# Optimization experiments

Measured on AMD Instinct MI355X. Metric: run time of the kernel, lower is better.

## Reference

```python
import jax, jax.numpy as jnp
import numpy as np

EMBED = 256      # embedding_dim
HEADS = 4        # attn_heads
OUT = EMBED // HEADS  # out_channels per head = 64
R = 8            # n_relations = len(metapaths) + 1
N = 16384        # num_nodes
NEG_SLOPE = 0.2  # PyG GATv2 default leaky_relu slope


def setup_inputs() -> dict:
    key = jax.random.key(0)
    ks = jax.random.split(key, 16)
    s = 0.05
    inp = {"relation_embs": jax.random.normal(ks[0], (N, R, EMBED), jnp.float32)}
    # Two GATv2Conv layers: lin_l (src), lin_r (dst), att vector, output bias.
    for i in range(2):
        inp[f"Wl{i}"] = jax.random.normal(ks[1 + 6 * i], (EMBED, HEADS, OUT), jnp.float32) * s
        inp[f"bl{i}"] = jax.random.normal(ks[2 + 6 * i], (HEADS, OUT), jnp.float32) * s
        inp[f"Wr{i}"] = jax.random.normal(ks[3 + 6 * i], (EMBED, HEADS, OUT), jnp.float32) * s
        inp[f"br{i}"] = jax.random.normal(ks[4 + 6 * i], (HEADS, OUT), jnp.float32) * s
        inp[f"att{i}"] = jax.random.normal(ks[5 + 6 * i], (HEADS, OUT), jnp.float32) * s
        inp[f"bias{i}"] = jax.random.normal(ks[6 + 6 * i], (HEADS * OUT,), jnp.float32) * s
    return inp


def reference(relation_embs, Wl0, bl0, Wr0, br0, att0, bias0,
              Wl1, bl1, Wr1, br1, att1, bias1):
    # Each node owns a fully-connected graph over its R relation embeddings
    # (all rows nonzero under randn fill), so the PyG gather/softmax/scatter
    # collapses to dense [N, R_dst, R_src] attention.
    h = jax.nn.relu(relation_embs)                                  # [N,R,D]

    # ---- GATv2 layer 0: full FC edges (every src -> every dst) ----
    xl = jnp.einsum('nrd,dhc->nrhc', h, Wl0) + bl0                  # src feats [N,R,H,C]
    xr = jnp.einsum('nrd,dhc->nrhc', h, Wr0) + br0                  # dst feats [N,R,H,C]
    e = jax.nn.leaky_relu(xr[:, :, None] + xl[:, None], NEG_SLOPE)  # [N,Ri,Rj,H,C]
    logits = jnp.einsum('nijhc,hc->nijh', e, att0)                  # [N,Ri,Rj,H]
    alpha = jax.nn.softmax(logits, axis=2)                          # softmax over src j
    h = jnp.einsum('nijh,njhc->nihc', alpha, xl)                    # [N,R,H,C]
    h = h.reshape(N, R, HEADS * OUT) + bias0
    h = jax.nn.relu(h)

    # ---- GATv2 layer 1 (last): only edges into the self node (nid == R-1) ----
    xl = jnp.einsum('nrd,dhc->nrhc', h, Wl1) + bl1                  # src feats [N,R,H,C]
    xr_self = jnp.einsum('nd,dhc->nhc', h[:, -1], Wr1) + br1        # dst = self [N,H,C]
    e = jax.nn.leaky_relu(xr_self[:, None] + xl, NEG_SLOPE)         # [N,R,H,C]
    logits = jnp.einsum('nrhc,hc->nrh', e, att1)                    # [N,R,H]
    alpha = jax.nn.softmax(logits, axis=1)                          # softmax over src r
    out = jnp.einsum('nrh,nrhc->nhc', alpha, xl).reshape(N, HEADS * OUT) + bias1
    node_embs = jax.nn.relu(out)                                    # [N, D]

    # betas: last-layer attention into the self node, detached (SparseTensor.to_dense().detach())
    betas = jax.lax.stop_gradient(alpha)                            # [N,R,H]
    return node_embs, betas
```

## Files before the change

kernel.cpp:

```cpp
#include <hip/hip_runtime.h>


#define NNODES 16384
#define NB 8
#define MR 64

typedef __bf16 bf16x8 __attribute__((ext_vector_type(8)));
typedef __bf16 bf16x4 __attribute__((ext_vector_type(4)));
typedef float f32x4 __attribute__((ext_vector_type(4)));
typedef float f32x8 __attribute__((ext_vector_type(8)));

__device__ __forceinline__ int swz(int row, int chunk) {
    return row * 256 + ((chunk ^ (row & 7)) << 3);
}

__global__ void prep_weights(const float* __restrict__ Wl0, const float* __restrict__ Wr0,
                             const float* __restrict__ Wl1, const float* __restrict__ Wr1,
                             __bf16* __restrict__ wt) {
    __shared__ float tile[64 * 68];
    const int t  = threadIdx.x;
    const int m  = blockIdx.x >> 4;
    const int kt = (blockIdx.x >> 2) & 3;
    const int nt = blockIdx.x & 3;
    const float* src = (m == 0 ? Wl0 : m == 1 ? Wr0 : m == 2 ? Wl1 : Wr1) + kt * 64 * 256;
    #pragma unroll
    for (int i = 0; i < 4; ++i) {
        const int idx = i * 256 + t;
        const int kk  = idx >> 4;
        const int nn  = (idx & 15) * 4;
        const float4 v = *(const float4*)&src[kk * 256 + nt * 64 + nn];
        tile[kk * 68 + nn + 0] = v.x;
        tile[kk * 68 + nn + 1] = v.y;
        tile[kk * 68 + nn + 2] = v.z;
        tile[kk * 68 + nn + 3] = v.w;
    }
    __syncthreads();
    const int n  = t >> 2;
    const int ks = (t & 3) * 16;
    bf16x8 o0, o1;
    #pragma unroll
    for (int e = 0; e < 8; ++e) o0[e] = (__bf16)tile[(ks + e) * 68 + n];
    #pragma unroll
    for (int e = 0; e < 8; ++e) o1[e] = (__bf16)tile[(ks + 8 + e) * 68 + n];
    __bf16* dst = &wt[(size_t)(m * 256 + nt * 64 + n) * 256 + kt * 64 + ks];
    *(bf16x8*)dst = o0;
    *(bf16x8*)(dst + 8) = o1;
}

__launch_bounds__(512, 4)
__global__ void gat_fused(const float* __restrict__ x,
                          const float* __restrict__ bl0, const float* __restrict__ br0,
                          const float* __restrict__ att0, const float* __restrict__ bias0,
                          const float* __restrict__ bl1, const float* __restrict__ br1,
                          const float* __restrict__ att1, const float* __restrict__ bias1,
                          const __bf16* __restrict__ wt,
                          float* __restrict__ out) {
    __shared__ __bf16 bufA[MR * 256];
    __shared__ __bf16 bufB[MR * 256];
    __shared__ float attbuf[2560];

    const int tid  = threadIdx.x;
    const int bg   = blockIdx.x;
    const int lane = tid & 63;
    const int wv   = tid >> 6;
    const int lr   = lane & 15;
    const int lq   = lane >> 4;

    {
        const float4* src = (const float4*)(x + (size_t)bg * (MR * 256));
        #pragma unroll
        for (int it = 0; it < 4; ++it) {
            const int g   = it * 512 + tid;
            const int row = g >> 5;
            const int c   = g & 31;
            const float4 v0 = src[2 * g];
            const float4 v1 = src[2 * g + 1];
            bf16x8 s;
            s[0] = (__bf16)fmaxf(v0.x, 0.f); s[1] = (__bf16)fmaxf(v0.y, 0.f);
            s[2] = (__bf16)fmaxf(v0.z, 0.f); s[3] = (__bf16)fmaxf(v0.w, 0.f);
            s[4] = (__bf16)fmaxf(v1.x, 0.f); s[5] = (__bf16)fmaxf(v1.y, 0.f);
            s[6] = (__bf16)fmaxf(v1.z, 0.f); s[7] = (__bf16)fmaxf(v1.w, 0.f);
            *(bf16x8*)&bufA[swz(row, c)] = s;
        }
        if (tid < 256) attbuf[2048 + tid] = att0[tid];
        else           attbuf[2048 + tid] = att1[tid - 256];
    }
    __syncthreads();

    {
        f32x4 acc[4][4];
        #pragma unroll
        for (int m = 0; m < 4; ++m)
            #pragma unroll
            for (int n = 0; n < 4; ++n)
                acc[m][n] = f32x4{0.f, 0.f, 0.f, 0.f};
        #pragma unroll
        for (int kt = 0; kt < 8; ++kt) {
            bf16x8 a[4], b[4];
            #pragma unroll
            for (int m = 0; m < 4; ++m)
                a[m] = *(const bf16x8*)&bufA[swz(m * 16 + lr, kt * 4 + lq)];
            const int koff = kt * 32 + lq * 8;
            #pragma unroll
            for (int n = 0; n < 4; ++n)
                b[n] = *(const bf16x8*)&wt[(size_t)(wv * 64 + n * 16 + lr) * 256 + koff];
            #pragma unroll
            for (int m = 0; m < 4; ++m)
                #pragma unroll
                for (int n = 0; n < 4; ++n)
                    acc[m][n] = __builtin_amdgcn_mfma_f32_16x16x32_bf16(a[m], b[n], acc[m][n], 0, 0, 0);
        }
        __syncthreads();
        __bf16* dstbuf = (wv < 4) ? bufB : bufA;
        const float* bv = (wv < 4) ? bl0 : br0;
        #pragma unroll
        for (int n = 0; n < 4; ++n) {
            const int cl   = (wv & 3) * 64 + n * 16 + lr;
            const float bias = bv[cl];
            const int ch   = cl >> 3, ce = cl & 7;
            #pragma unroll
            for (int m = 0; m < 4; ++m)
                #pragma unroll
                for (int r = 0; r < 4; ++r) {
                    const int row = m * 16 + lq * 4 + r;
                    dstbuf[swz(row, ch) + ce] = (__bf16)(acc[m][n][r] + bias);
                }
        }
    }
    __syncthreads();

    {
        const int n  = tid >> 6;
        const int i  = (tid >> 3) & 7;
        const int h  = (tid >> 1) & 3;
        const int jh = tid & 1;
        const int rowR = n * 8 + i;
        float lg[4] = {0.f, 0.f, 0.f, 0.f};
        #pragma unroll
        for (int cc = 0; cc < 8; ++cc) {
            const bf16x8 vr = *(const bf16x8*)&bufA[swz(rowR, h * 8 + cc)];
            const f32x8 xr = __builtin_convertvector(vr, f32x8);
            const float4 a0 = *(const float4*)&attbuf[2048 + h * 64 + cc * 8];
            const float4 a1 = *(const float4*)&attbuf[2048 + h * 64 + cc * 8 + 4];
            const float av[8] = {a0.x, a0.y, a0.z, a0.w, a1.x, a1.y, a1.z, a1.w};
            #pragma unroll
            for (int jj = 0; jj < 4; ++jj) {
                const int rowL = n * 8 + jh * 4 + jj;
                const bf16x8 vl = *(const bf16x8*)&bufB[swz(rowL, h * 8 + cc)];
                const f32x8 xl = __builtin_convertvector(vl, f32x8);
                #pragma unroll
                for (int e = 0; e < 8; ++e) {
                    float t = xr[e] + xl[e];
                    t = fmaxf(t, 0.2f * t);
                    lg[jj] = fmaf(t, av[e], lg[jj]);
                }
            }
        }
        float mx = fmaxf(fmaxf(lg[0], lg[1]), fmaxf(lg[2], lg[3]));
        mx = fmaxf(mx, __shfl_xor(mx, 1));
        float ex[4], ssum = 0.f;
        #pragma unroll
        for (int jj = 0; jj < 4; ++jj) { ex[jj] = __expf(lg[jj] - mx); ssum += ex[jj]; }
        const float tot = ssum + __shfl_xor(ssum, 1);
        const float inv = 1.f / tot;
        #pragma unroll
        for (int jj = 0; jj < 4; ++jj)
            attbuf[((n * 8 + i) * 4 + h) * 8 + jh * 4 + jj] = ex[jj] * inv;
    }
    __syncthreads();

    {
        const int row  = tid >> 3;
        const int sub  = tid & 7;
        const int h    = sub >> 1;
        const int half = sub & 1;
        const int cb   = h * 8 + half * 4;
        const int nn   = row >> 3;
        float alpha[8];
        #pragma unroll
        for (int j = 0; j < 8; ++j) alpha[j] = attbuf[(row * 4 + h) * 8 + j];
        float o[32];
        #pragma unroll
        for (int c = 0; c < 32; ++c) o[c] = 0.f;
        #pragma unroll
        for (int j = 0; j < 8; ++j) {
            const int rowj = nn * 8 + j;
            #pragma unroll
            for (int cc = 0; cc < 4; ++cc) {
                const bf16x8 v = *(const bf16x8*)&bufB[swz(rowj, cb + cc)];
                const f32x8 f = __builtin_convertvector(v, f32x8);
                #pragma unroll
                for (int e = 0; e < 8; ++e)
                    o[cc * 8 + e] = fmaf(f[e], alpha[j], o[cc * 8 + e]);
            }
        }
        #pragma unroll
        for (int cc = 0; cc < 4; ++cc) {
            bf16x8 s;
            #pragma unroll
            for (int e = 0; e < 8; ++e) {
                const float v = o[cc * 8 + e] + bias0[(cb + cc) * 8 + e];
                s[e] = (__bf16)fmaxf(v, 0.f);
            }
            *(bf16x8*)&bufA[swz(row, cb + cc)] = s;
        }
    }
    __syncthreads();

    {
        f32x4 accl[4][2], accr[2];
        #pragma unroll
        for (int m = 0; m < 4; ++m)
            #pragma unroll
            for (int n = 0; n < 2; ++n)
                accl[m][n] = f32x4{0.f, 0.f, 0.f, 0.f};
        #pragma unroll
        for (int n = 0; n < 2; ++n) accr[n] = f32x4{0.f, 0.f, 0.f, 0.f};
        const __bf16* W1l = wt + 512 * 256;
        const __bf16* W1r = wt + 768 * 256;
        const int rowS = (lr & 7) * 8 + 7;
        #pragma unroll
        for (int kt = 0; kt < 8; ++kt) {
            const int koff = kt * 32 + lq * 8;
            bf16x8 a[4], as, bl[2], br[2];
            #pragma unroll
            for (int m = 0; m < 4; ++m)
                a[m] = *(const bf16x8*)&bufA[swz(m * 16 + lr, kt * 4 + lq)];
            as = *(const bf16x8*)&bufA[swz(rowS, kt * 4 + lq)];
            #pragma unroll
            for (int n = 0; n < 2; ++n) {
                bl[n] = *(const bf16x8*)&W1l[(size_t)(wv * 32 + n * 16 + lr) * 256 + koff];
                br[n] = *(const bf16x8*)&W1r[(size_t)(wv * 32 + n * 16 + lr) * 256 + koff];
            }
            #pragma unroll
            for (int m = 0; m < 4; ++m)
                #pragma unroll
                for (int n = 0; n < 2; ++n)
                    accl[m][n] = __builtin_amdgcn_mfma_f32_16x16x32_bf16(a[m], bl[n], accl[m][n], 0, 0, 0);
            #pragma unroll
            for (int n = 0; n < 2; ++n)
                accr[n] = __builtin_amdgcn_mfma_f32_16x16x32_bf16(as, br[n], accr[n], 0, 0, 0);
        }
        #pragma unroll
        for (int n = 0; n < 2; ++n) {
            const int col = wv * 32 + n * 16 + lr;
            const float b1 = bl1[col], b2 = br1[col];
            const int ch = col >> 3, ce = col & 7;
            #pragma unroll
            for (int m = 0; m < 4; ++m)
                #pragma unroll
                for (int r = 0; r < 4; ++r) {
                    const int row = m * 16 + lq * 4 + r;
                    bufB[swz(row, ch) + ce] = (__bf16)(accl[m][n][r] + b1);
                }
            if (lq < 2) {
                #pragma unroll
                for (int r = 0; r < 4; ++r) {
                    const int node = lq * 4 + r;
                    attbuf[node * 256 + col] = accr[n][r] + b2;
                }
            }
        }
    }
    __syncthreads();

    {
        const int n  = tid >> 5;
        const int rr = (tid >> 2) & 7;
        const int h  = tid & 3;
        float lg = 0.f;
        if (tid < 256) {
            const int rowj = n * 8 + rr;
            #pragma unroll
            for (int cc = 0; cc < 8; ++cc) {
                const float4 r0 = *(const float4*)&attbuf[n * 256 + h * 64 + cc * 8];
                const float4 r1 = *(const float4*)&attbuf[n * 256 + h * 64 + cc * 8 + 4];
                const float xr[8] = {r0.x, r0.y, r0.z, r0.w, r1.x, r1.y, r1.z, r1.w};
                const bf16x8 vl = *(const bf16x8*)&bufB[swz(rowj, h * 8 + cc)];
                const f32x8 xl = __builtin_convertvector(vl, f32x8);
                const float4 a0 = *(const float4*)&attbuf[2304 + h * 64 + cc * 8];
                const float4 a1 = *(const float4*)&attbuf[2304 + h * 64 + cc * 8 + 4];
                const float av[8] = {a0.x, a0.y, a0.z, a0.w, a1.x, a1.y, a1.z, a1.w};
                #pragma unroll
                for (int e = 0; e < 8; ++e) {
                    float t = xr[e] + xl[e];
                    t = fmaxf(t, 0.2f * t);
                    lg = fmaf(t, av[e], lg);
                }
            }
        }
        __syncthreads();
        if (tid < 256) attbuf[2048 + tid] = lg;
        __syncthreads();
        if (tid < 256) {
            float M = -1e30f;
            float l[8];
            #pragma unroll
            for (int j = 0; j < 8; ++j) {
                l[j] = attbuf[2048 + n * 32 + j * 4 + h];
                M = fmaxf(M, l[j]);
            }
            float S = 0.f;
            #pragma unroll
            for (int j = 0; j < 8; ++j) S += __expf(l[j] - M);
            const float a = __expf(lg - M) / S;
            attbuf[tid] = a;
            out[(size_t)NNODES * 256 + (size_t)(bg * NB + n) * 32 + rr * 4 + h] = a;
        }
    }
    __syncthreads();

    {
        const int n  = tid >> 6;
        const int q  = tid & 63;
        const int c0 = q * 4;
        const int h  = q >> 4;
        float o0 = 0.f, o1 = 0.f, o2 = 0.f, o3 = 0.f;
        #pragma unroll
        for (int r = 0; r < 8; ++r) {
            const float a = attbuf[n * 32 + r * 4 + h];
            const int rowj = n * 8 + r;
            const bf16x4 v = *(const bf16x4*)&bufB[swz(rowj, q >> 1) + (q & 1) * 4];
            o0 = fmaf((float)v[0], a, o0);
            o1 = fmaf((float)v[1], a, o1);
            o2 = fmaf((float)v[2], a, o2);
            o3 = fmaf((float)v[3], a, o3);
        }
        float4 res;
        res.x = fmaxf(o0 + bias1[c0 + 0], 0.f);
        res.y = fmaxf(o1 + bias1[c0 + 1], 0.f);
        res.z = fmaxf(o2 + bias1[c0 + 2], 0.f);
        res.w = fmaxf(o3 + bias1[c0 + 3], 0.f);
        *(float4*)&out[(size_t)(bg * NB + n) * 256 + c0] = res;
    }
}

extern "C" void kernel_launch(void* const* d_in, const int* in_sizes, int n_in,
                              void* d_out, int out_size, void* d_ws, size_t ws_size,
                              hipStream_t stream) {
    const float* x     = (const float*)d_in[0];
    const float* Wl0   = (const float*)d_in[1];
    const float* bl0   = (const float*)d_in[2];
    const float* Wr0   = (const float*)d_in[3];
    const float* br0   = (const float*)d_in[4];
    const float* att0  = (const float*)d_in[5];
    const float* bias0 = (const float*)d_in[6];
    const float* Wl1   = (const float*)d_in[7];
    const float* bl1   = (const float*)d_in[8];
    const float* Wr1   = (const float*)d_in[9];
    const float* br1   = (const float*)d_in[10];
    const float* att1  = (const float*)d_in[11];
    const float* bias1 = (const float*)d_in[12];
    __bf16* wt = (__bf16*)d_ws;
    float* out = (float*)d_out;

    prep_weights<<<64, 256, 0, stream>>>(Wl0, Wr0, Wl1, Wr1, wt);
    gat_fused<<<NNODES / NB, 512, 0, stream>>>(x, bl0, br0, att0, bias0,
                                               bl1, br1, att1, bias1, wt, out);
}
```

Measured before the change: 369.5 us.

## Switch intermediates to fp16 and use packed half math with fdot2 for attention

Replaces bf16 storage and MFMA with fp16 throughout, so attention logits and aggregation can run in packed f16x2 arithmetic. Logits use packed add, packed leaky-relu and fdot2 instead of scalar fp32 FMAs, and layer-0 aggregation accumulates in packed half. Attention vectors and bias0 are staged as fp16 in shared memory, and chunk indices are rotated per head to spread LDS bank accesses. The aim is to cut VALU instruction count in the elementwise attention stages, at the cost of fp16 range limits and reduced accumulation precision.

After: 353.1 us. -4.4%, faster.

```diff
diff --git a/kernel.cpp b/kernel.cpp
--- a/kernel.cpp
+++ b/kernel.cpp
@@ -5,10 +5,40 @@
 #define NB 8
 #define MR 64
 
-typedef __bf16 bf16x8 __attribute__((ext_vector_type(8)));
-typedef __bf16 bf16x4 __attribute__((ext_vector_type(4)));
+typedef _Float16 f16x8 __attribute__((ext_vector_type(8)));
+typedef _Float16 f16x4 __attribute__((ext_vector_type(4)));
+typedef _Float16 f16x2 __attribute__((ext_vector_type(2)));
 typedef float f32x4 __attribute__((ext_vector_type(4)));
-typedef float f32x8 __attribute__((ext_vector_type(8)));
+
+#if __has_builtin(__builtin_amdgcn_fdot2)
+#define FDOT2(a, b, c) __builtin_amdgcn_fdot2((a), (b), (c), false)
+#else
+#define FDOT2(a, b, c) ((c) + (float)(a)[0] * (float)(b)[0] + (float)(a)[1] * (float)(b)[1])
+#endif
+
+__device__ __forceinline__ f16x2 pk2(float a, float b) {
+    return __builtin_bit_cast(f16x2, __builtin_amdgcn_cvt_pkrtz(a, b));
+}
+
+__device__ __forceinline__ f16x2 leaky2(f16x2 t) {
+#if __has_builtin(__builtin_elementwise_max)
+    return __builtin_elementwise_max(t, t * (f16x2){(_Float16)0.2f, (_Float16)0.2f});
+#else
+    const unsigned u = __builtin_bit_cast(unsigned, t) & 0x7FFF7FFFu;
+    const f16x2 at = __builtin_bit_cast(f16x2, u);
+    return t * (f16x2){(_Float16)0.6f, (_Float16)0.6f} +
+           at * (f16x2){(_Float16)0.4f, (_Float16)0.4f};
+#endif
+}
+__device__ __forceinline__ f16x2 relu2(f16x2 t) {
+#if __has_builtin(__builtin_elementwise_max)
+    return __builtin_elementwise_max(t, (f16x2){(_Float16)0.f, (_Float16)0.f});
+#else
+    const unsigned u = __builtin_bit_cast(unsigned, t) & 0x7FFF7FFFu;
+    const f16x2 at = __builtin_bit_cast(f16x2, u);
+    return (t + at) * (f16x2){(_Float16)0.5f, (_Float16)0.5f};
+#endif
+}
 
 __device__ __forceinline__ int swz(int row, int chunk) {
     return row * 256 + ((chunk ^ (row & 7)) << 3);
@@ -16,7 +46,7 @@
 
 __global__ void prep_weights(const float* __restrict__ Wl0, const float* __restrict__ Wr0,
                              const float* __restrict__ Wl1, const float* __restrict__ Wr1,
-                             __bf16* __restrict__ wt) {
+                             _Float16* __restrict__ wt) {
     __shared__ float tile[64 * 68];
     const int t  = threadIdx.x;
     const int m  = blockIdx.x >> 4;
@@ -37,14 +67,14 @@
     __syncthreads();
     const int n  = t >> 2;
     const int ks = (t & 3) * 16;
-    bf16x8 o0, o1;
+    f16x8 o0, o1;
     #pragma unroll
-    for (int e = 0; e < 8; ++e) o0[e] = (__bf16)tile[(ks + e) * 68 + n];
+    for (int e = 0; e < 8; ++e) o0[e] = (_Float16)tile[(ks + e) * 68 + n];
     #pragma unroll
-    for (int e = 0; e < 8; ++e) o1[e] = (__bf16)tile[(ks + 8 + e) * 68 + n];
-    __bf16* dst = &wt[(size_t)(m * 256 + nt * 64 + n) * 256 + kt * 64 + ks];
-    *(bf16x8*)dst = o0;
-    *(bf16x8*)(dst + 8) = o1;
+    for (int e = 0; e < 8; ++e) o1[e] = (_Float16)tile[(ks + 8 + e) * 68 + n];
+    _Float16* dst = &wt[(size_t)(m * 256 + nt * 64 + n) * 256 + kt * 64 + ks];
+    *(f16x8*)dst = o0;
+    *(f16x8*)(dst + 8) = o1;
 }
 
 __launch_bounds__(512, 4)
@@ -53,11 +83,12 @@
                           const float* __restrict__ att0, const float* __restrict__ bias0,
                           const float* __restrict__ bl1, const float* __restrict__ br1,
                           const float* __restrict__ att1, const float* __restrict__ bias1,
-                          const __bf16* __restrict__ wt,
+                          const _Float16* __restrict__ wt,
                           float* __restrict__ out) {
-    __shared__ __bf16 bufA[MR * 256];
-    __shared__ __bf16 bufB[MR * 256];
-    __shared__ float attbuf[2560];
+    __shared__ _Float16 bufA[MR * 256];
+    __shared__ _Float16 bufB[MR * 256];
+    __shared__ float attbuf[2304];
+    __shared__ _Float16 attH[768];
 
     const int tid  = threadIdx.x;
     const int bg   = blockIdx.x;
@@ -75,15 +106,19 @@
             const int c   = g & 31;
             const float4 v0 = src[2 * g];
             const float4 v1 = src[2 * g + 1];
-            bf16x8 s;
-            s[0] = (__bf16)fmaxf(v0.x, 0.f); s[1] = (__bf16)fmaxf(v0.y, 0.f);
-            s[2] = (__bf16)fmaxf(v0.z, 0.f); s[3] = (__bf16)fmaxf(v0.w, 0.f);
-            s[4] = (__bf16)fmaxf(v1.x, 0.f); s[5] = (__bf16)fmaxf(v1.y, 0.f);
-            s[6] = (__bf16)fmaxf(v1.z, 0.f); s[7] = (__bf16)fmaxf(v1.w, 0.f);
-            *(bf16x8*)&bufA[swz(row, c)] = s;
-        }
-        if (tid < 256) attbuf[2048 + tid] = att0[tid];
-        else           attbuf[2048 + tid] = att1[tid - 256];
+            f16x8 s;
+            s[0] = (_Float16)fmaxf(v0.x, 0.f); s[1] = (_Float16)fmaxf(v0.y, 0.f);
+            s[2] = (_Float16)fmaxf(v0.z, 0.f); s[3] = (_Float16)fmaxf(v0.w, 0.f);
+            s[4] = (_Float16)fmaxf(v1.x, 0.f); s[5] = (_Float16)fmaxf(v1.y, 0.f);
+            s[6] = (_Float16)fmaxf(v1.z, 0.f); s[7] = (_Float16)fmaxf(v1.w, 0.f);
+            *(f16x8*)&bufA[swz(row, c)] = s;
+        }
+        if (tid < 256) {
+            attH[tid]       = (_Float16)att0[tid];
+            attH[512 + tid] = (_Float16)bias0[tid];
+        } else {
+            attH[tid]       = (_Float16)att1[tid - 256];
+        }
     }
     __syncthreads();
 
@@ -96,22 +131,22 @@
                 acc[m][n] = f32x4{0.f, 0.f, 0.f, 0.f};
         #pragma unroll
         for (int kt = 0; kt < 8; ++kt) {
-            bf16x8 a[4], b[4];
-            #pragma unroll
-            for (int m = 0; m < 4; ++m)
-                a[m] = *(const bf16x8*)&bufA[swz(m * 16 + lr, kt * 4 + lq)];
+            f16x8 a[4], b[4];
+            #pragma unroll
+            for (int m = 0; m < 4; ++m)
+                a[m] = *(const f16x8*)&bufA[swz(m * 16 + lr, kt * 4 + lq)];
             const int koff = kt * 32 + lq * 8;
             #pragma unroll
             for (int n = 0; n < 4; ++n)
-                b[n] = *(const bf16x8*)&wt[(size_t)(wv * 64 + n * 16 + lr) * 256 + koff];
+                b[n] = *(const f16x8*)&wt[(size_t)(wv * 64 + n * 16 + lr) * 256 + koff];
             #pragma unroll
             for (int m = 0; m < 4; ++m)
                 #pragma unroll
                 for (int n = 0; n < 4; ++n)
-                    acc[m][n] = __builtin_amdgcn_mfma_f32_16x16x32_bf16(a[m], b[n], acc[m][n], 0, 0, 0);
+                    acc[m][n] = __builtin_amdgcn_mfma_f32_16x16x32_f16(a[m], b[n], acc[m][n], 0, 0, 0);
         }
         __syncthreads();
-        __bf16* dstbuf = (wv < 4) ? bufB : bufA;
+        _Float16* dstbuf = (wv < 4) ? bufB : bufA;
         const float* bv = (wv < 4) ? bl0 : br0;
         #pragma unroll
         for (int n = 0; n < 4; ++n) {
@@ -123,7 +158,7 @@
                 #pragma unroll
                 for (int r = 0; r < 4; ++r) {
                     const int row = m * 16 + lq * 4 + r;
-                    dstbuf[swz(row, ch) + ce] = (__bf16)(acc[m][n][r] + bias);
+                    dstbuf[swz(row, ch) + ce] = (_Float16)(acc[m][n][r] + bias);
                 }
         }
     }
@@ -135,24 +170,31 @@
         const int h  = (tid >> 1) & 3;
         const int jh = tid & 1;
         const int rowR = n * 8 + i;
+        f16x2 xr2[32];
+        #pragma unroll
+        for (int cc = 0; cc < 8; ++cc) {
+            const int c3 = (cc + 2 * h) & 7;
+            const f16x8 v = *(const f16x8*)&bufA[swz(rowR, h * 8 + c3)];
+            xr2[cc * 4 + 0] = f16x2{v[0], v[1]};
+            xr2[cc * 4 + 1] = f16x2{v[2], v[3]};
+            xr2[cc * 4 + 2] = f16x2{v[4], v[5]};
+            xr2[cc * 4 + 3] = f16x2{v[6], v[7]};
+        }
         float lg[4] = {0.f, 0.f, 0.f, 0.f};
         #pragma unroll
         for (int cc = 0; cc < 8; ++cc) {
-            const bf16x8 vr = *(const bf16x8*)&bufA[swz(rowR, h * 8 + cc)];
-            const f32x8 xr = __builtin_convertvector(vr, f32x8);
-            const float4 a0 = *(const float4*)&attbuf[2048 + h * 64 + cc * 8];
-            const float4 a1 = *(const float4*)&attbuf[2048 + h * 64 + cc * 8 + 4];
-            const float av[8] = {a0.x, a0.y, a0.z, a0.w, a1.x, a1.y, a1.z, a1.w};
+            const int c3 = (cc + 2 * h) & 7;
+            const f16x8 a8 = *(const f16x8*)&attH[h * 64 + c3 * 8];
+            const f16x2 a2[4] = {{a8[0], a8[1]}, {a8[2], a8[3]}, {a8[4], a8[5]}, {a8[6], a8[7]}};
             #pragma unroll
             for (int jj = 0; jj < 4; ++jj) {
                 const int rowL = n * 8 + jh * 4 + jj;
-                const bf16x8 vl = *(const bf16x8*)&bufB[swz(rowL, h * 8 + cc)];
-                const f32x8 xl = __builtin_convertvector(vl, f32x8);
-                #pragma unroll
-                for (int e = 0; e < 8; ++e) {
-                    float t = xr[e] + xl[e];
-                    t = fmaxf(t, 0.2f * t);
-                    lg[jj] = fmaf(t, av[e], lg[jj]);
+                const f16x8 l8 = *(const f16x8*)&bufB[swz(rowL, h * 8 + c3)];
+                const f16x2 l2[4] = {{l8[0], l8[1]}, {l8[2], l8[3]}, {l8[4], l8[5]}, {l8[6], l8[7]}};
+                #pragma unroll
+                for (int p = 0; p < 4; ++p) {
+                    const f16x2 t = leaky2(xr2[cc * 4 + p] + l2[p]);
+                    lg[jj] = FDOT2(t, a2[p], lg[jj]);
                 }
             }
         }
@@ -174,35 +216,37 @@
         const int sub  = tid & 7;
         const int h    = sub >> 1;
         const int half = sub & 1;
-        const int cb   = h * 8 + half * 4;
         const int nn   = row >> 3;
-        float alpha[8];
-        #pragma unroll
-        for (int j = 0; j < 8; ++j) alpha[j] = attbuf[(row * 4 + h) * 8 + j];
-        float o[32];
-        #pragma unroll
-        for (int c = 0; c < 32; ++c) o[c] = 0.f;
+        f16x2 acc2[16];
+        #pragma unroll
+        for (int p = 0; p < 16; ++p) acc2[p] = (f16x2){(_Float16)0.f, (_Float16)0.f};
         #pragma unroll
         for (int j = 0; j < 8; ++j) {
+            const _Float16 ah = (_Float16)attbuf[(row * 4 + h) * 8 + j];
+            const f16x2 a2 = {ah, ah};
             const int rowj = nn * 8 + j;
             #pragma unroll
             for (int cc = 0; cc < 4; ++cc) {
-                const bf16x8 v = *(const bf16x8*)&bufB[swz(rowj, cb + cc)];
-                const f32x8 f = __builtin_convertvector(v, f32x8);
-                #pragma unroll
-                for (int e = 0; e < 8; ++e)
-                    o[cc * 8 + e] = fmaf(f[e], alpha[j], o[cc * 8 + e]);
+                const int c = h * 8 + half * 4 + ((cc + h) & 3);
+                const f16x8 v = *(const f16x8*)&bufB[swz(rowj, c)];
+                acc2[cc * 4 + 0] += f16x2{v[0], v[1]} * a2;
+                acc2[cc * 4 + 1] += f16x2{v[2], v[3]} * a2;
+                acc2[cc * 4 + 2] += f16x2{v[4], v[5]} * a2;
+                acc2[cc * 4 + 3] += f16x2{v[6], v[7]} * a2;
             }
         }
         #pragma unroll
         for (int cc = 0; cc < 4; ++cc) {
-            bf16x8 s;
-            #pragma unroll
-            for (int e = 0; e < 8; ++e) {
-                const float v = o[cc * 8 + e] + bias0[(cb + cc) * 8 + e];
-                s[e] = (__bf16)fmaxf(v, 0.f);
-            }
-            *(bf16x8*)&bufA[swz(row, cb + cc)] = s;
+            const int c = h * 8 + half * 4 + ((cc + h) & 3);
+            const f16x8 b8 = *(const f16x8*)&attH[512 + c * 8];
+            f16x8 s;
+            #pragma unroll
+            for (int p = 0; p < 4; ++p) {
+                const f16x2 r = relu2(acc2[cc * 4 + p] + f16x2{b8[2 * p], b8[2 * p + 1]});
+                s[2 * p]     = r[0];
+                s[2 * p + 1] = r[1];
+            }
+            *(f16x8*)&bufA[swz(row, c)] = s;
         }
     }
     __syncthreads();
@@ -216,30 +260,30 @@
                 accl[m][n] = f32x4{0.f, 0.f, 0.f, 0.f};
         #pragma unroll
         for (int n = 0; n < 2; ++n) accr[n] = f32x4{0.f, 0.f, 0.f, 0.f};
-        const __bf16* W1l = wt + 512 * 256;
-        const __bf16* W1r = wt + 768 * 256;
+        const _Float16* W1l = wt + 512 * 256;
+        const _Float16* W1r = wt + 768 * 256;
         const int rowS = (lr & 7) * 8 + 7;
         #pragma unroll
         for (int kt = 0; kt < 8; ++kt) {
             const int koff = kt * 32 + lq * 8;
-            bf16x8 a[4], as, bl[2], br[2];
-            #pragma unroll
-            for (int m = 0; m < 4; ++m)
-                a[m] = *(const bf16x8*)&bufA[swz(m * 16 + lr, kt * 4 + lq)];
-            as = *(const bf16x8*)&bufA[swz(rowS, kt * 4 + lq)];
+            f16x8 a[4], as, bl[2], br[2];
+            #pragma unroll
+            for (int m = 0; m < 4; ++m)
+                a[m] = *(const f16x8*)&bufA[swz(m * 16 + lr, kt * 4 + lq)];
+            as = *(const f16x8*)&bufA[swz(rowS, kt * 4 + lq)];
             #pragma unroll
             for (int n = 0; n < 2; ++n) {
-                bl[n] = *(const bf16x8*)&W1l[(size_t)(wv * 32 + n * 16 + lr) * 256 + koff];
-                br[n] = *(const bf16x8*)&W1r[(size_t)(wv * 32 + n * 16 + lr) * 256 + koff];
+                bl[n] = *(const f16x8*)&W1l[(size_t)(wv * 32 + n * 16 + lr) * 256 + koff];
+                br[n] = *(const f16x8*)&W1r[(size_t)(wv * 32 + n * 16 + lr) * 256 + koff];
             }
             #pragma unroll
             for (int m = 0; m < 4; ++m)
                 #pragma unroll
                 for (int n = 0; n < 2; ++n)
-                    accl[m][n] = __builtin_amdgcn_mfma_f32_16x16x32_bf16(a[m], bl[n], accl[m][n], 0, 0, 0);
+                    accl[m][n] = __builtin_amdgcn_mfma_f32_16x16x32_f16(a[m], bl[n], accl[m][n], 0, 0, 0);
             #pragma unroll
             for (int n = 0; n < 2; ++n)
-                accr[n] = __builtin_amdgcn_mfma_f32_16x16x32_bf16(as, br[n], accr[n], 0, 0, 0);
+                accr[n] = __builtin_amdgcn_mfma_f32_16x16x32_f16(as, br[n], accr[n], 0, 0, 0);
         }
         #pragma unroll
         for (int n = 0; n < 2; ++n) {
@@ -251,7 +295,7 @@
                 #pragma unroll
                 for (int r = 0; r < 4; ++r) {
                     const int row = m * 16 + lq * 4 + r;
-                    bufB[swz(row, ch) + ce] = (__bf16)(accl[m][n][r] + b1);
+                    bufB[swz(row, ch) + ce] = (_Float16)(accl[m][n][r] + b1);
                 }
             if (lq < 2) {
                 #pragma unroll
@@ -273,19 +317,20 @@
             const int rowj = n * 8 + rr;
             #pragma unroll
             for (int cc = 0; cc < 8; ++cc) {
-                const float4 r0 = *(const float4*)&attbuf[n * 256 + h * 64 + cc * 8];
-                const float4 r1 = *(const float4*)&attbuf[n * 256 + h * 64 + cc * 8 + 4];
-                const float xr[8] = {r0.x, r0.y, r0.z, r0.w, r1.x, r1.y, r1.z, r1.w};
-                const bf16x8 vl = *(const bf16x8*)&bufB[swz(rowj, h * 8 + cc)];
-                const f32x8 xl = __builtin_convertvector(vl, f32x8);
-                const float4 a0 = *(const float4*)&attbuf[2304 + h * 64 + cc * 8];
-                const float4 a1 = *(const float4*)&attbuf[2304 + h * 64 + cc * 8 + 4];
-                const float av[8] = {a0.x, a0.y, a0.z, a0.w, a1.x, a1.y, a1.z, a1.w};
-                #pragma unroll
-                for (int e = 0; e < 8; ++e) {
-                    float t = xr[e] + xl[e];
-                    t = fmaxf(t, 0.2f * t);
-                    lg = fmaf(t, av[e], lg);
+                const int c3 = (cc + 2 * h) & 7;
+                const int c  = h * 8 + c3;
+                const float4 r0 = *(const float4*)&attbuf[n * 256 + c * 8];
+                const float4 r1 = *(const float4*)&attbuf[n * 256 + c * 8 + 4];
+                const f16x2 x2[4] = {pk2(r0.x, r0.y), pk2(r0.z, r0.w),
+                                     pk2(r1.x, r1.y), pk2(r1.z, r1.w)};
+                const f16x8 l8 = *(const f16x8*)&bufB[swz(rowj, c)];
+                const f16x2 l2[4] = {{l8[0], l8[1]}, {l8[2], l8[3]}, {l8[4], l8[5]}, {l8[6], l8[7]}};
+                const f16x8 a8 = *(const f16x8*)&attH[256 + c * 8];
+                const f16x2 a2[4] = {{a8[0], a8[1]}, {a8[2], a8[3]}, {a8[4], a8[5]}, {a8[6], a8[7]}};
+                #pragma unroll
+                for (int p = 0; p < 4; ++p) {
+                    const f16x2 t = leaky2(x2[p] + l2[p]);
+                    lg = FDOT2(t, a2[p], lg);
                 }
             }
         }
@@ -320,7 +365,7 @@
         for (int r = 0; r < 8; ++r) {
             const float a = attbuf[n * 32 + r * 4 + h];
             const int rowj = n * 8 + r;
-            const bf16x4 v = *(const bf16x4*)&bufB[swz(rowj, q >> 1) + (q & 1) * 4];
+            const f16x4 v = *(const f16x4*)&bufB[swz(rowj, q >> 1) + (q & 1) * 4];
             o0 = fmaf((float)v[0], a, o0);
             o1 = fmaf((float)v[1], a, o1);
             o2 = fmaf((float)v[2], a, o2);
@@ -351,7 +396,7 @@
     const float* br1   = (const float*)d_in[10];
     const float* att1  = (const float*)d_in[11];
     const float* bias1 = (const float*)d_in[12];
-    __bf16* wt = (__bf16*)d_ws;
+    _Float16* wt = (_Float16*)d_ws;
     float* out = (float*)d_out;
 
     prep_weights<<<64, 256, 0, stream>>>(Wl0, Wr0, Wl1, Wr1, wt);
```
